# Performance work log

Measured on AMD Instinct MI355X. Metric: run time of the kernel, lower is better.

## Reference

```python
import jax, jax.numpy as jnp
import numpy as np

U, S, T = 3000, 1500, 32
B = 16384
MAX_NEIGHBORS = 50


def setup_inputs() -> dict:
    key = jax.random.key(0)
    k1, k2, k3, k4, k5, k6 = jax.random.split(key, 6)
    qos_matrix = jax.random.uniform(k1, (U, S, T), dtype=jnp.float32)
    mask_matrix = jax.random.randint(k2, (U, S, T), 0, 2) > 0
    qos_matrix = jnp.where(mask_matrix, qos_matrix, 0.0)
    # avg_qos consistent with module's precomputed per-(user,service) mean
    cnt = mask_matrix.sum(axis=2)
    avg_qos = jnp.where(cnt > 0, qos_matrix.sum(axis=2) / jnp.maximum(cnt, 1), 0.0).astype(jnp.float32)
    user_sim = jax.random.uniform(k3, (U, U), minval=-1.0, maxval=1.0, dtype=jnp.float32)
    user_sim = (user_sim + user_sim.T) * 0.5
    user_sim = user_sim.at[jnp.arange(U), jnp.arange(U)].set(1.0)
    time_ids = jax.random.randint(k4, (B,), 0, T)
    user_ids = jax.random.randint(k5, (B,), 0, U)
    service_ids = jax.random.randint(k6, (B,), 0, S)
    return {"qos_matrix": qos_matrix, "mask_matrix": mask_matrix, "avg_qos": avg_qos,
            "user_sim": user_sim, "time_ids": time_ids, "user_ids": user_ids,
            "service_ids": service_ids}


def reference(qos_matrix, mask_matrix, avg_qos, user_sim, time_ids, user_ids, service_ids):
    # base QoS estimate per sample: [B]
    base = avg_qos[user_ids, service_ids]
    # top-k similar users for each query user: [B, K]
    sims = user_sim[user_ids]                      # [B, U]
    topk_val, topk_idx = jax.lax.top_k(sims, MAX_NEIGHBORS)
    s_col = service_ids[:, None]                   # [B, 1]
    t_col = time_ids[:, None]
    valid = mask_matrix[topk_idx, s_col, t_col]    # [B, K] bool
    w = jnp.where(valid, topk_val, 0.0)            # zero out unobserved neighbors
    dev = qos_matrix[topk_idx, s_col, t_col] - avg_qos[topk_idx, s_col]  # [B, K]
    dev_sum = (w * dev).sum(axis=-1)
    sim_sum = w.sum(axis=-1)
    safe = jnp.where(sim_sum > 0, sim_sum, 1.0)
    deviation = jnp.where(sim_sum > 0, dev_sum / safe, 0.0)
    return jnp.maximum(base + deviation, 0.0)
```

## Files before the change

### kernel.cpp

```cpp
#include <hip/hip_runtime.h>

#define UU 3000
#define SS 1500
#define TT 32
#define BB 16384
#define KK 50

__global__ __launch_bounds__(256) void detect_mask(const unsigned int* __restrict__ mask,
                                                   int* __restrict__ flag) {
    __shared__ int bad_i32, bad_f32;
    if (threadIdx.x == 0) { bad_i32 = 0; bad_f32 = 0; }
    __syncthreads();
    for (int i = threadIdx.x; i < 4096; i += 256) {
        unsigned int w = mask[i];
        if (w > 1u) bad_i32 = 1;
        if (w != 0u && w != 0x3F800000u) bad_f32 = 1;
    }
    __syncthreads();
    if (threadIdx.x == 0) {
        int f = 0;
        if (bad_i32) f = bad_f32 ? 1 : 2;
        *flag = f;
    }
}

__global__ __launch_bounds__(256) void topk_kernel(const float* __restrict__ user_sim,
                                                   int* __restrict__ topk_idx,
                                                   float* __restrict__ topk_val) {
    __shared__ unsigned long long keys[UU];
    __shared__ unsigned long long wmax[4];
    const int u = blockIdx.x;
    const float* row = user_sim + (size_t)u * UU;

    for (int i = threadIdx.x; i < UU; i += 256) {
        unsigned int b = __float_as_uint(row[i]);
        b = (b & 0x80000000u) ? ~b : (b | 0x80000000u);
        keys[i] = ((unsigned long long)b << 32) | (unsigned int)(0xFFFFFFFFu - (unsigned int)i);
    }
    __syncthreads();

    for (int k = 0; k < KK; ++k) {
        unsigned long long best = 0ull;
        for (int i = threadIdx.x; i < UU; i += 256) {
            unsigned long long v = keys[i];
            best = (v > best) ? v : best;
        }
        for (int m = 32; m >= 1; m >>= 1) {
            unsigned long long o = __shfl_xor(best, m, 64);
            best = (o > best) ? o : best;
        }
        if ((threadIdx.x & 63) == 0) wmax[threadIdx.x >> 6] = best;
        __syncthreads();
        if (threadIdx.x == 0) {
            best = wmax[0];
            for (int w = 1; w < 4; ++w) best = (wmax[w] > best) ? wmax[w] : best;
            unsigned int idx = 0xFFFFFFFFu - (unsigned int)(best & 0xFFFFFFFFull);
            unsigned int ub  = (unsigned int)(best >> 32);
            float f = (ub & 0x80000000u) ? __uint_as_float(ub & 0x7FFFFFFFu)
                                         : __uint_as_float(~ub);
            topk_idx[u * KK + k] = (int)idx;
            topk_val[u * KK + k] = f;
            keys[idx] = 0ull;
        }
        __syncthreads();
    }
}

__global__ __launch_bounds__(256) void gather_kernel(
    const float* __restrict__ qos, const void* __restrict__ mask,
    const float* __restrict__ avg, const int* __restrict__ time_ids,
    const int* __restrict__ user_ids, const int* __restrict__ service_ids,
    const int* __restrict__ topk_idx, const float* __restrict__ topk_val,
    const int* __restrict__ flag, float* __restrict__ out) {

    const int wave = (int)((blockIdx.x * blockDim.x + threadIdx.x) >> 6);
    const int lane = (int)(threadIdx.x & 63);
    if (wave >= BB) return;

    const int u = user_ids[wave];
    const int s = service_ids[wave];
    const int t = time_ids[wave];
    const float base = avg[(size_t)u * SS + s];
    const int fl = *flag;

    float wv = 0.0f, dv = 0.0f;
    if (lane < KK) {
        const int   idx = topk_idx[u * KK + lane];
        const float val = topk_val[u * KK + lane];
        const size_t off3 = ((size_t)idx * SS + s) * TT + t;
        int m;
        if (fl == 0)       m = ((const int*)mask)[off3];
        else if (fl == 1)  m = (int)((const unsigned char*)mask)[off3];
        else               m = (((const float*)mask)[off3] != 0.0f) ? 1 : 0;
        if (m) {
            const float q = qos[off3];
            const float a = avg[(size_t)idx * SS + s];
            wv = val;
            dv = val * (q - a);
        }
    }
    for (int m2 = 32; m2 >= 1; m2 >>= 1) {
        wv += __shfl_xor(wv, m2, 64);
        dv += __shfl_xor(dv, m2, 64);
    }
    if (lane == 0) {
        const float deviation = (wv > 0.0f) ? (dv / wv) : 0.0f;
        const float r = base + deviation;
        out[wave] = (r > 0.0f) ? r : 0.0f;
    }
}

extern "C" void kernel_launch(void* const* d_in, const int* in_sizes, int n_in,
                              void* d_out, int out_size, void* d_ws, size_t ws_size,
                              hipStream_t stream) {
    const float* qos      = (const float*)d_in[0];
    const void*  mask     = d_in[1];
    const float* avg      = (const float*)d_in[2];
    const float* user_sim = (const float*)d_in[3];
    const int* time_ids    = (const int*)d_in[4];
    const int* user_ids    = (const int*)d_in[5];
    const int* service_ids = (const int*)d_in[6];
    float* out = (float*)d_out;

    int*   topk_idx = (int*)d_ws;
    float* topk_val = (float*)((char*)d_ws + (size_t)UU * KK * 4);
    int*   flag     = (int*)((char*)d_ws + (size_t)UU * KK * 8);

    detect_mask<<<1, 256, 0, stream>>>((const unsigned int*)mask, flag);
    topk_kernel<<<UU, 256, 0, stream>>>(user_sim, topk_idx, topk_val);
    gather_kernel<<<(BB * 64) / 256, 256, 0, stream>>>(
        qos, mask, avg, time_ids, user_ids, service_ids,
        topk_idx, topk_val, flag, out);
}
```

Before: 1.059 ms.

## Replace iterative argmax top-k with radix-select and hoist gather loads

Top-k selection per user row is changed from 50 sequential block-wide argmax reductions to a 4-pass 8-bit radix select over 32-bit keys. Elements above the threshold are emitted directly and ties are resolved by lowest index. The gather kernel now issues the qos and avg loads unconditionally instead of after the mask check, so they can overlap with the mask load. This trades fewer barriers and reductions for shared-memory atomics, extra loads for masked-out neighbours, and an unordered neighbour list.

```diff
diff --git a/kernel.cpp b/kernel.cpp
--- a/kernel.cpp
+++ b/kernel.cpp
@@ -24,45 +24,103 @@
     }
 }
 
-__global__ __launch_bounds__(256) void topk_kernel(const float* __restrict__ user_sim,
+__device__ __forceinline__ unsigned int float_to_key(float f) {
+    unsigned int b = __float_as_uint(f);
+    return (b & 0x80000000u) ? ~b : (b | 0x80000000u);
+}
+__device__ __forceinline__ float key_to_float(unsigned int k) {
+    return (k & 0x80000000u) ? __uint_as_float(k & 0x7FFFFFFFu)
+                             : __uint_as_float(~k);
+}
+
+__global__ __launch_bounds__(256) void topk_select(const float* __restrict__ user_sim,
                                                    int* __restrict__ topk_idx,
                                                    float* __restrict__ topk_val) {
-    __shared__ unsigned long long keys[UU];
-    __shared__ unsigned long long wmax[4];
+    __shared__ unsigned int keys[UU];
+    __shared__ int hist[256];
+    __shared__ int s_bin, s_rem;
+    __shared__ int cnt_gt, eq_cnt;
+    __shared__ int eq_list[64];
+
     const int u = blockIdx.x;
     const float* row = user_sim + (size_t)u * UU;
 
+    for (int i = threadIdx.x; i < UU; i += 256)
+        keys[i] = float_to_key(row[i]);
+    if (threadIdx.x == 0) { cnt_gt = 0; eq_cnt = 0; }
+
+    unsigned int prefix = 0u, prefmask = 0u;
+    int remaining = KK;
+
+    for (int pass = 0; pass < 4; ++pass) {
+        const int shift = 24 - pass * 8;
+        hist[threadIdx.x] = 0;
+        __syncthreads();
+        for (int i = threadIdx.x; i < UU; i += 256) {
+            unsigned int k = keys[i];
+            if ((k & prefmask) == prefix)
+                atomicAdd(&hist[(k >> shift) & 0xFFu], 1);
+        }
+        __syncthreads();
+        if (threadIdx.x < 64) {
+            const int lane = threadIdx.x;
+            const int h0 = hist[4 * lane + 0], h1 = hist[4 * lane + 1];
+            const int h2 = hist[4 * lane + 2], h3 = hist[4 * lane + 3];
+            const int local = h0 + h1 + h2 + h3;
+            int x = local;
+            for (int off = 1; off < 64; off <<= 1) {
+                int y = __shfl_down(x, off, 64);
+                if (lane + off < 64) x += y;
+            }
+            const int excl = x - local;
+            if (excl < remaining && remaining <= excl + local) {
+                int acc = excl;
+                const int hs[4] = { h3, h2, h1, h0 };
+                const int bo[4] = { 3, 2, 1, 0 };
+                for (int j = 0; j < 4; ++j) {
+                    if (acc + hs[j] >= remaining) {
+                        s_bin = 4 * lane + bo[j];
+                        s_rem = remaining - acc;
+                        break;
+                    }
+                    acc += hs[j];
+                }
+            }
+        }
+        __syncthreads();
+        prefix  |= ((unsigned int)s_bin) << shift;
+        prefmask |= (0xFFu << shift);
+        remaining = s_rem;
+        __syncthreads();
+    }
+
+    const unsigned int thr = prefix;
     for (int i = threadIdx.x; i < UU; i += 256) {
-        unsigned int b = __float_as_uint(row[i]);
-        b = (b & 0x80000000u) ? ~b : (b | 0x80000000u);
-        keys[i] = ((unsigned long long)b << 32) | (unsigned int)(0xFFFFFFFFu - (unsigned int)i);
+        unsigned int k = keys[i];
+        if (k > thr) {
+            int p = atomicAdd(&cnt_gt, 1);
+            topk_idx[u * KK + p] = i;
+            topk_val[u * KK + p] = key_to_float(k);
+        } else if (k == thr) {
+            int e = atomicAdd(&eq_cnt, 1);
+            if (e < 64) eq_list[e] = i;
+        }
     }
     __syncthreads();
-
-    for (int k = 0; k < KK; ++k) {
-        unsigned long long best = 0ull;
-        for (int i = threadIdx.x; i < UU; i += 256) {
-            unsigned long long v = keys[i];
-            best = (v > best) ? v : best;
+    if (threadIdx.x == 0) {
+        const int n = eq_cnt < 64 ? eq_cnt : 64;
+        const float fv = key_to_float(thr);
+        const int base = KK - remaining;
+        for (int r = 0; r < remaining; ++r) {
+            int mi = -1, mv = 0x7FFFFFFF;
+            for (int j = 0; j < n; ++j) {
+                int v = eq_list[j];
+                if (v >= 0 && v < mv) { mv = v; mi = j; }
+            }
+            eq_list[mi] = -1;
+            topk_idx[u * KK + base + r] = mv;
+            topk_val[u * KK + base + r] = fv;
         }
-        for (int m = 32; m >= 1; m >>= 1) {
-            unsigned long long o = __shfl_xor(best, m, 64);
-            best = (o > best) ? o : best;
-        }
-        if ((threadIdx.x & 63) == 0) wmax[threadIdx.x >> 6] = best;
-        __syncthreads();
-        if (threadIdx.x == 0) {
-            best = wmax[0];
-            for (int w = 1; w < 4; ++w) best = (wmax[w] > best) ? wmax[w] : best;
-            unsigned int idx = 0xFFFFFFFFu - (unsigned int)(best & 0xFFFFFFFFull);
-            unsigned int ub  = (unsigned int)(best >> 32);
-            float f = (ub & 0x80000000u) ? __uint_as_float(ub & 0x7FFFFFFFu)
-                                         : __uint_as_float(~ub);
-            topk_idx[u * KK + k] = (int)idx;
-            topk_val[u * KK + k] = f;
-            keys[idx] = 0ull;
-        }
-        __syncthreads();
     }
 }
 
@@ -88,16 +146,14 @@
         const int   idx = topk_idx[u * KK + lane];
         const float val = topk_val[u * KK + lane];
         const size_t off3 = ((size_t)idx * SS + s) * TT + t;
+        const float q = qos[off3];
+        const float a = avg[(size_t)idx * SS + s];
         int m;
         if (fl == 0)       m = ((const int*)mask)[off3];
         else if (fl == 1)  m = (int)((const unsigned char*)mask)[off3];
         else               m = (((const float*)mask)[off3] != 0.0f) ? 1 : 0;
-        if (m) {
-            const float q = qos[off3];
-            const float a = avg[(size_t)idx * SS + s];
-            wv = val;
-            dv = val * (q - a);
-        }
+        wv = m ? val : 0.0f;
+        dv = m ? val * (q - a) : 0.0f;
     }
     for (int m2 = 32; m2 >= 1; m2 >>= 1) {
         wv += __shfl_xor(wv, m2, 64);
@@ -127,7 +183,7 @@
     int*   flag     = (int*)((char*)d_ws + (size_t)UU * KK * 8);
 
     detect_mask<<<1, 256, 0, stream>>>((const unsigned int*)mask, flag);
-    topk_kernel<<<UU, 256, 0, stream>>>(user_sim, topk_idx, topk_val);
+    topk_select<<<UU, 256, 0, stream>>>(user_sim, topk_idx, topk_val);
     gather_kernel<<<(BB * 64) / 256, 256, 0, stream>>>(
         qos, mask, avg, time_ids, user_ids, service_ids,
         topk_idx, topk_val, flag, out);
```

Measured after the change: 947.9 us. -10.5%, faster.
